# Optimization experiments

Hardware: AMD Instinct MI355X
Metric: run time of the kernel (lower is better)

## Reference

```python
import jax, jax.numpy as jnp
import numpy as np

EPS = 1e-10
N_NODES = 100000
OUT_CH = 128
N_EDGES = 625000


def setup_inputs() -> dict:
    key = jax.random.key(0)
    k_emb, k_eidx, k_enorm, k_lw, k_sw = jax.random.split(key, 5)
    emb = jax.random.normal(k_emb, (N_NODES, OUT_CH), dtype=jnp.float32) * 0.02
    edge_index = jax.random.randint(k_eidx, (2, N_EDGES), 0, N_NODES, dtype=jnp.int64)
    edge_norm = jax.random.uniform(k_enorm, (N_EDGES,), dtype=jnp.float32)
    scale = 1.0 / np.sqrt(OUT_CH)
    loc_w = jax.random.normal(k_lw, (OUT_CH, OUT_CH), dtype=jnp.float32) * scale
    loc_b = jnp.zeros((OUT_CH,), dtype=jnp.float32)
    std_w = jax.random.normal(k_sw, (OUT_CH, OUT_CH), dtype=jnp.float32) * scale
    std_b = jnp.zeros((OUT_CH,), dtype=jnp.float32)
    return {"emb": emb, "edge_index": edge_index, "edge_norm": edge_norm,
            "loc_w": loc_w, "loc_b": loc_b, "std_w": std_w, "std_b": std_b}


def reference(emb, edge_index, edge_norm, loc_w, loc_b, std_w, std_b):
    """GraphEncoder (GraphConv gather-scale-scatter + Linear loc/std) followed by
    GraphDecoder dot-product logits on the same edge list. Eval mode: z = loc."""
    sidx = edge_index[0]
    tidx = edge_index[1]
    # GraphConv: message = x[sidx] * enorm ; scatter_add into target nodes
    message = emb[sidx] * edge_norm[:, None]               # [E, C]
    ptr = jax.ops.segment_sum(message, tidx, num_segments=emb.shape[0])  # [N, C]
    # Encoder heads (torch Linear: x @ W.T + b)
    loc = ptr @ loc_w.T + loc_b                            # [N, C]
    std = jax.nn.softplus(ptr @ std_w.T + std_b) + EPS     # [N, C]
    z = loc  # eval-mode embedding
    # GraphDecoder: Bernoulli logits per edge
    logits = jnp.sum(z[sidx] * z[tidx], axis=1)            # [E]
    return loc, std, logits
```

## Files before the change

### kernel.cpp

```cpp
#include <hip/hip_runtime.h>

#define N_NODES 100000
#define OUT_CH  128
#define N_EDGES 625000
#define NB_SCAN 98
#define ROWD 68

typedef short short8 __attribute__((ext_vector_type(8)));
typedef float f32x4  __attribute__((ext_vector_type(4)));
typedef float f32x2  __attribute__((ext_vector_type(2)));
typedef unsigned u32x4 __attribute__((ext_vector_type(4)));

__device__ inline short f32_bf16(float f) {
    union { float f; unsigned u; } c{f};
    unsigned r = 0x7FFFu + ((c.u >> 16) & 1u);
    return (short)((c.u + r) >> 16);
}
__device__ inline unsigned pack_bf16x2(float lo, float hi) {
    return (unsigned)(unsigned short)f32_bf16(lo) |
           ((unsigned)(unsigned short)f32_bf16(hi) << 16);
}
__device__ inline float sp_fast(float x) {
    float e = __expf(-fabsf(x));
    return fmaxf(x, 0.f) + __logf(1.f + e);
}

#if defined(__has_builtin)
#if __has_builtin(__builtin_amdgcn_cvt_pk_f32_fp8) && __has_builtin(__builtin_amdgcn_cvt_pk_fp8_f32)
#define HWFP8 1
#endif
#endif
#ifndef HWFP8
#define HWFP8 0
#endif

__device__ inline unsigned f32_fp8_manual(float f) {
    union { float fl; unsigned u; } c{f};
    unsigned s = (c.u >> 31) << 7;
    float af = fabsf(f);
    if (!(af < 448.f)) return s | 0x7E;
    if (af < 0.015625f) {
        unsigned q = (unsigned)__float2int_rn(af * 512.f);
        return s | q;
    }
    unsigned u = c.u;
    u += 0x7FFFF + ((u >> 20) & 1);
    int e = (int)((u >> 23) & 255) - 127;
    if (e > 8) return s | 0x7E;
    return s | (((unsigned)(e + 7)) << 3) | ((u >> 20) & 7);
}
__device__ inline float fp8_f32_manual(unsigned b) {
    unsigned s = (b >> 7) & 1, e = (b >> 3) & 15, m = b & 7;
    if (e) { union { unsigned u; float f; } c{(s << 31) | ((e + 120) << 23) | (m << 20)}; return c.f; }
    float v = (float)m * 0.001953125f;
    return s ? -v : v;
}

template <bool HI>
__device__ inline f32x2 fp8x2_f32(unsigned v) {
#if HWFP8
    return __builtin_amdgcn_cvt_pk_f32_fp8((int)v, HI);
#else
    unsigned sh = HI ? 16 : 0;
    f32x2 r;
    r.x = fp8_f32_manual((v >> sh) & 0xff);
    r.y = fp8_f32_manual((v >> (sh + 8)) & 0xff);
    return r;
#endif
}
template <bool HI>
__device__ inline unsigned fp8_pack2(float a, float b, unsigned old) {
#if HWFP8
    return (unsigned)__builtin_amdgcn_cvt_pk_fp8_f32(a, b, (int)old, HI);
#else
    unsigned v = f32_fp8_manual(a) | (f32_fp8_manual(b) << 8);
    return HI ? ((old & 0x0000ffffu) | (v << 16)) : ((old & 0xffff0000u) | v);
#endif
}

#define NBB 16
#define NBE 6250
#define NBH 2442
__global__ void prep_all(const float* __restrict__ lw, const float* __restrict__ sw,
                         short8* __restrict__ B, const float4* __restrict__ emb,
                         uint2* __restrict__ embf8, const int* __restrict__ ei,
                         int* __restrict__ counts, int use_fp8) {
    int bid = blockIdx.x, tid = threadIdx.x;
    if (bid < NBB) {
        int g = bid * 256 + tid;
        int lane = g & 63, nt = (g >> 6) & 15, ks = g >> 10;
        int c = nt * 16 + (lane & 15);
        int k = ks * 32 + (lane >> 4) * 8;
        const float* src = (c < OUT_CH) ? (lw + c * OUT_CH + k)
                                        : (sw + (c - OUT_CH) * OUT_CH + k);
        short8 o;
#pragma unroll
        for (int j = 0; j < 8; ++j) o[j] = f32_bf16(src[j]);
        B[(ks * 16 + nt) * 64 + lane] = o;
    } else if (bid < NBB + NBE) {
        if (!use_fp8) return;
        int i = (bid - NBB) * 256 + tid;
        float4 a = emb[2 * i], b = emb[2 * i + 1];
        unsigned lo = fp8_pack2<false>(a.x * 64.f, a.y * 64.f, 0u);
        lo = fp8_pack2<true>(a.z * 64.f, a.w * 64.f, lo);
        unsigned hi = fp8_pack2<false>(b.x * 64.f, b.y * 64.f, 0u);
        hi = fp8_pack2<true>(b.z * 64.f, b.w * 64.f, hi);
        uint2 o; o.x = lo; o.y = hi;
        embf8[i] = o;
    } else {
        int e = (bid - NBB - NBE) * 256 + tid;
        if (e < N_EDGES) atomicAdd(&counts[ei[N_EDGES + e]], 1);
    }
}

__global__ void scan1_k(const int* __restrict__ counts, int* __restrict__ offsets,
                        int* __restrict__ partials, int* __restrict__ cursors) {
    __shared__ int wsum[16];
    int tid = threadIdx.x, lane = tid & 63, wid = tid >> 6;
    int e = blockIdx.x * 1024 + tid;
    int v = (e < N_NODES) ? counts[e] : 0;
    int incl = v;
#pragma unroll
    for (int d = 1; d < 64; d <<= 1) {
        int t = __shfl_up(incl, d);
        if (lane >= d) incl += t;
    }
    if (lane == 63) wsum[wid] = incl;
    __syncthreads();
    if (wid == 0) {
        int w = (lane < 16) ? wsum[lane] : 0;
        int wi = w;
#pragma unroll
        for (int d = 1; d < 16; d <<= 1) {
            int t = __shfl_up(wi, d);
            if (lane >= d) wi += t;
        }
        if (lane < 16) wsum[lane] = wi - w;
        if (lane == 15) partials[blockIdx.x] = wi;
    }
    __syncthreads();
    int excl = incl - v + wsum[wid];
    if (e < N_NODES) { offsets[e] = excl; cursors[e] = excl; }
}

__global__ void scan2_k(int* __restrict__ partials, int nb) {
    int lane = threadIdx.x;
    int i0 = 2 * lane, i1 = 2 * lane + 1;
    int v0 = (i0 < nb) ? partials[i0] : 0;
    int v1 = (i1 < nb) ? partials[i1] : 0;
    int s = v0 + v1;
    int incl = s;
#pragma unroll
    for (int d = 1; d < 64; d <<= 1) {
        int t = __shfl_up(incl, d);
        if (lane >= d) incl += t;
    }
    int excl = incl - s;
    if (i0 < nb) partials[i0] = excl;
    if (i1 < nb) partials[i1] = excl + v0;
}

__global__ void reorder_k(const int* __restrict__ ei, const float* __restrict__ en,
                          const int* __restrict__ partials, int* __restrict__ cursors,
                          int4* __restrict__ edata, float nscale) {
    int e = blockIdx.x * blockDim.x + threadIdx.x;
    if (e >= N_EDGES) return;
    int t = ei[N_EDGES + e];
    int pos = partials[t >> 10] + atomicAdd(&cursors[t], 1);
    int4 d;
    d.x = ei[e];
    d.y = __float_as_int(en[e] * nscale);
    d.z = e;
    d.w = t;
    edata[pos] = d;
}

__global__ __launch_bounds__(1024) void enc_fp8_k(
        const unsigned short* __restrict__ embf8,
        const int* __restrict__ offsets, const int* __restrict__ partials,
        const int4* __restrict__ edata, const short8* __restrict__ B,
        const float* __restrict__ lb, const float* __restrict__ sb,
        float* __restrict__ out, unsigned* __restrict__ zf8) {
    __shared__ unsigned lds[16 * ROWD];
    int tid = threadIdx.x, wid = tid >> 6, lane = tid & 63;
    int node = __builtin_amdgcn_readfirstlane(blockIdx.x * 16 + wid);

    int beg = offsets[node] + partials[node >> 10];
    int end = (node == N_NODES - 1) ? N_EDGES
              : offsets[node + 1] + partials[(node + 1) >> 10];
    float ax = 0.f, ay = 0.f;
    int j = beg;
    for (; j + 4 <= end; j += 4) {
        int4 p0 = edata[j], p1 = edata[j + 1], p2 = edata[j + 2], p3 = edata[j + 3];
        unsigned v0 = embf8[(size_t)p0.x * 64 + lane];
        unsigned v1 = embf8[(size_t)p1.x * 64 + lane];
        unsigned v2 = embf8[(size_t)p2.x * 64 + lane];
        unsigned v3 = embf8[(size_t)p3.x * 64 + lane];
        float n0f = __int_as_float(p0.y), n1f = __int_as_float(p1.y);
        float n2f = __int_as_float(p2.y), n3f = __int_as_float(p3.y);
        f32x2 d0 = fp8x2_f32<false>(v0), d1 = fp8x2_f32<false>(v1);
        f32x2 d2 = fp8x2_f32<false>(v2), d3 = fp8x2_f32<false>(v3);
        ax += d0.x * n0f + d1.x * n1f + d2.x * n2f + d3.x * n3f;
        ay += d0.y * n0f + d1.y * n1f + d2.y * n2f + d3.y * n3f;
    }
    for (; j < end; ++j) {
        int4 p = edata[j];
        float nm = __int_as_float(p.y);
        f32x2 d = fp8x2_f32<false>(embf8[(size_t)p.x * 64 + lane]);
        ax += d.x * nm; ay += d.y * nm;
    }
    lds[wid * ROWD + lane] = pack_bf16x2(ax, ay);
    __syncthreads();

    int arow = lane & 15, hi = lane >> 4;
    f32x4 acc = (f32x4)(0.f);
#pragma unroll
    for (int ks = 0; ks < 4; ++ks) {
        short8 a = *(const short8*)&lds[arow * ROWD + ks * 16 + hi * 4];
        short8 w = B[(ks * 16 + wid) * 64 + lane];
        acc = __builtin_amdgcn_mfma_f32_16x16x32_bf16(w, a, acc, 0, 0, 0);
    }
    int onode = blockIdx.x * 16 + arow;
    int ch4 = hi * 4;
    if (wid < 8) {
        int c = wid * 16 + ch4;
        float4 b4 = *(const float4*)(lb + c);
        float4 v;
        v.x = acc[0] + b4.x; v.y = acc[1] + b4.y;
        v.z = acc[2] + b4.z; v.w = acc[3] + b4.w;
        *(float4*)(out + (size_t)onode * OUT_CH + c) = v;
        unsigned zp = fp8_pack2<false>(v.x * 16.f, v.y * 16.f, 0u);
        zp = fp8_pack2<true>(v.z * 16.f, v.w * 16.f, zp);
        zf8[(size_t)onode * 32 + (c >> 2)] = zp;
    } else {
        int cc = (wid - 8) * 16 + ch4;
        float4 b4 = *(const float4*)(sb + cc);
        float4 v;
        v.x = sp_fast(acc[0] + b4.x) + 1e-10f;
        v.y = sp_fast(acc[1] + b4.y) + 1e-10f;
        v.z = sp_fast(acc[2] + b4.z) + 1e-10f;
        v.w = sp_fast(acc[3] + b4.w) + 1e-10f;
        *(float4*)(out + (size_t)N_NODES * OUT_CH + (size_t)onode * OUT_CH + cc) = v;
    }
}

__global__ void gather_f32_k(const float* __restrict__ emb,
                             const int* __restrict__ offsets,
                             const int* __restrict__ partials,
                             const int4* __restrict__ edata,
                             unsigned* __restrict__ ptrb) {
    int g = blockIdx.x * blockDim.x + threadIdx.x;
    int node = __builtin_amdgcn_readfirstlane(g >> 6);
    int lane = threadIdx.x & 63;
    if (node >= N_NODES) return;
    int beg = offsets[node] + partials[node >> 10];
    int end = (node == N_NODES - 1) ? N_EDGES
              : offsets[node + 1] + partials[(node + 1) >> 10];
    float ax = 0.f, ay = 0.f;
    const float2* base = (const float2*)emb;
    int j = beg;
    for (; j + 4 <= end; j += 4) {
        int4 p0 = edata[j], p1 = edata[j + 1], p2 = edata[j + 2], p3 = edata[j + 3];
        float2 v0 = base[(size_t)p0.x * 64 + lane];
        float2 v1 = base[(size_t)p1.x * 64 + lane];
        float2 v2 = base[(size_t)p2.x * 64 + lane];
        float2 v3 = base[(size_t)p3.x * 64 + lane];
        float n0f = __int_as_float(p0.y), n1f = __int_as_float(p1.y);
        float n2f = __int_as_float(p2.y), n3f = __int_as_float(p3.y);
        ax += v0.x * n0f + v1.x * n1f + v2.x * n2f + v3.x * n3f;
        ay += v0.y * n0f + v1.y * n1f + v2.y * n2f + v3.y * n3f;
    }
    for (; j < end; ++j) {
        int4 p = edata[j];
        float nm = __int_as_float(p.y);
        float2 v = base[(size_t)p.x * 64 + lane];
        ax += v.x * nm; ay += v.y * nm;
    }
    ptrb[(size_t)node * 64 + lane] = pack_bf16x2(ax, ay);
}

__global__ __launch_bounds__(256) void gemm_k(const short* __restrict__ P,
                                              float* __restrict__ out,
                                              const short8* __restrict__ B,
                                              const float* __restrict__ lb,
                                              const float* __restrict__ sb) {
    int tid = threadIdx.x;
    int wave = tid >> 6, lane = tid & 63;
    int n0 = (blockIdx.x * 4 + wave) * 16;
    if (n0 >= N_NODES) return;

    float* loc  = out;
    float* stdo = out + (size_t)N_NODES * OUT_CH;

    int prow = n0 + (lane & 15);
    int kb = (lane >> 4) * 8;

    f32x4 acc[16];
#pragma unroll
    for (int i = 0; i < 16; ++i) acc[i] = (f32x4)(0.f);

#pragma unroll
    for (int ks = 0; ks < 4; ++ks) {
        short8 a = *(const short8*)(P + (size_t)prow * OUT_CH + ks * 32 + kb);
#pragma unroll
        for (int nt = 0; nt < 16; ++nt) {
            short8 w = B[(ks * 16 + nt) * 64 + lane];
            acc[nt] = __builtin_amdgcn_mfma_f32_16x16x32_bf16(w, a, acc[nt], 0, 0, 0);
        }
    }

    int node = n0 + (lane & 15);
    int ch4 = (lane >> 4) * 4;
    float* lrow = loc  + (size_t)node * OUT_CH;
    float* srow = stdo + (size_t)node * OUT_CH;

#pragma unroll
    for (int nt = 0; nt < 8; ++nt) {
        int c = nt * 16 + ch4;
        float4 b4 = *(const float4*)(lb + c);
        float4 v;
        v.x = acc[nt][0] + b4.x; v.y = acc[nt][1] + b4.y;
        v.z = acc[nt][2] + b4.z; v.w = acc[nt][3] + b4.w;
        *(float4*)(lrow + c) = v;
    }
#pragma unroll
    for (int nt = 8; nt < 16; ++nt) {
        int cc = nt * 16 + ch4 - OUT_CH;
        float4 b4 = *(const float4*)(sb + cc);
        float4 v;
        v.x = sp_fast(acc[nt][0] + b4.x) + 1e-10f;
        v.y = sp_fast(acc[nt][1] + b4.y) + 1e-10f;
        v.z = sp_fast(acc[nt][2] + b4.z) + 1e-10f;
        v.w = sp_fast(acc[nt][3] + b4.w) + 1e-10f;
        *(float4*)(srow + cc) = v;
    }
}

__global__ void logits_fp8_k(const u32x4* __restrict__ zf8,
                             const int4* __restrict__ edata,
                             float* __restrict__ lg) {
    int idx = blockIdx.x * blockDim.x + threadIdx.x;
    int p = idx >> 3, q = idx & 7;
    if (p >= N_EDGES) return;
    int4 md = edata[p];
    u32x4 a = zf8[(size_t)md.x * 8 + q];
    u32x4 b = zf8[(size_t)md.w * 8 + q];
    float d = 0.f;
#pragma unroll
    for (int k = 0; k < 4; ++k) {
        f32x2 al = fp8x2_f32<false>(a[k]), ah = fp8x2_f32<true>(a[k]);
        f32x2 bl = fp8x2_f32<false>(b[k]), bh = fp8x2_f32<true>(b[k]);
        d += al.x * bl.x + al.y * bl.y + ah.x * bh.x + ah.y * bh.y;
    }
#pragma unroll
    for (int m = 4; m >= 1; m >>= 1) d += __shfl_xor(d, m);
    if (q == 0) lg[md.z] = d * 0.00390625f;
}

__global__ void logits_f32_k(const float* __restrict__ z, const int* __restrict__ ei,
                             float* __restrict__ lg) {
    int idx = blockIdx.x * blockDim.x + threadIdx.x;
    int e = idx >> 5, q = idx & 31;
    if (e >= N_EDGES) return;
    int s = ei[e], t = ei[N_EDGES + e];
    float4 a = *(const float4*)(z + (size_t)s * OUT_CH + q * 4);
    float4 b = *(const float4*)(z + (size_t)t * OUT_CH + q * 4);
    float d = a.x * b.x + a.y * b.y + a.z * b.z + a.w * b.w;
#pragma unroll
    for (int m = 16; m >= 1; m >>= 1) d += __shfl_xor(d, m);
    if (q == 0) lg[e] = d;
}

extern "C" void kernel_launch(void* const* d_in, const int* in_sizes, int n_in,
                              void* d_out, int out_size, void* d_ws, size_t ws_size,
                              hipStream_t stream) {
    const float* emb = (const float*)d_in[0];
    const int*   ei  = (const int*)d_in[1];
    const float* en  = (const float*)d_in[2];
    const float* lw  = (const float*)d_in[3];
    const float* lb  = (const float*)d_in[4];
    const float* sw  = (const float*)d_in[5];
    const float* sb  = (const float*)d_in[6];
    float* out = (float*)d_out;

    char* ws = (char*)d_ws;
    size_t o = 0;
    short8* B       = (short8*)(ws + o); o += 65536;
    int*    counts  = (int*)(ws + o);    o += 400128;
    int*    offsets = (int*)(ws + o);    o += 400128;
    int*    cursors = (int*)(ws + o);    o += 400128;
    int*    partials= (int*)(ws + o);    o += 1024;
    int4*   edata   = (int4*)(ws + o);   o += (size_t)N_EDGES * 16;
    unsigned* ptrb  = (unsigned*)(ws + o); o += (size_t)N_NODES * OUT_CH * 2;

    unsigned* zf8   = (unsigned*)(ws + o);
    unsigned short* embf8 = (unsigned short*)(ws + o + (size_t)N_NODES * OUT_CH);
    size_t o_end = o + (size_t)N_NODES * OUT_CH * 2;
    int use_fp8 = (o_end <= ws_size) ? 1 : 0;

    hipMemsetAsync(counts, 0, N_NODES * sizeof(int), stream);

    prep_all<<<NBB + NBE + NBH, 256, 0, stream>>>(lw, sw, B, (const float4*)emb,
                                                  (uint2*)embf8, ei, counts, use_fp8);
    scan1_k<<<NB_SCAN, 1024, 0, stream>>>(counts, offsets, partials, cursors);
    scan2_k<<<1, 64, 0, stream>>>(partials, NB_SCAN);
    reorder_k<<<(N_EDGES + 255) / 256, 256, 0, stream>>>(
        ei, en, partials, cursors, edata, use_fp8 ? 0.015625f : 1.0f);
    float* lg = out + (size_t)2 * N_NODES * OUT_CH;
    if (use_fp8) {
        enc_fp8_k<<<N_NODES / 16, 1024, 0, stream>>>(embf8, offsets, partials,
                                                     edata, B, lb, sb, out, zf8);
        logits_fp8_k<<<((size_t)N_EDGES * 8 + 255) / 256, 256, 0, stream>>>(
            (const u32x4*)zf8, edata, lg);
    } else {
        gather_f32_k<<<(N_NODES * 64 + 255) / 256, 256, 0, stream>>>(
            emb, offsets, partials, edata, ptrb);
        gemm_k<<<(N_NODES / 16 + 3) / 4, 256, 0, stream>>>((const short*)ptrb, out,
                                                           B, lb, sb);
        logits_f32_k<<<((size_t)N_EDGES * 32 + 255) / 256, 256, 0, stream>>>(out, ei, lg);
    }
}
```

Before: 177.0 us.

## Sort nodes by in-degree so encoder blocks process similar-degree nodes together

Builds a degree histogram during the scan, prefix-sums it, then scatters node IDs into degree-bucketed order. The fused encoder kernel now maps each wave to a node taken from this sorted list, so the 16 waves in a block have similar edge counts and finish at similar times before the shared MFMA step. The cost is an extra kernel, extra atomics, and output rows written in scattered order instead of contiguously.

```diff
diff --git a/kernel.cpp b/kernel.cpp
--- a/kernel.cpp
+++ b/kernel.cpp
@@ -114,11 +114,14 @@
 }
 
 __global__ void scan1_k(const int* __restrict__ counts, int* __restrict__ offsets,
-                        int* __restrict__ partials, int* __restrict__ cursors) {
+                        int* __restrict__ partials, int* __restrict__ cursors,
+                        int* __restrict__ dcur) {
     __shared__ int wsum[16];
+    __shared__ int lh[64];
     int tid = threadIdx.x, lane = tid & 63, wid = tid >> 6;
     int e = blockIdx.x * 1024 + tid;
     int v = (e < N_NODES) ? counts[e] : 0;
+    if (tid < 64) lh[tid] = 0;
     int incl = v;
 #pragma unroll
     for (int d = 1; d < 64; d <<= 1) {
@@ -127,6 +130,7 @@
     }
     if (lane == 63) wsum[wid] = incl;
     __syncthreads();
+    if (e < N_NODES) atomicAdd(&lh[v < 63 ? v : 63], 1);
     if (wid == 0) {
         int w = (lane < 16) ? wsum[lane] : 0;
         int wi = w;
@@ -141,9 +145,10 @@
     __syncthreads();
     int excl = incl - v + wsum[wid];
     if (e < N_NODES) { offsets[e] = excl; cursors[e] = excl; }
-}
-
-__global__ void scan2_k(int* __restrict__ partials, int nb) {
+    if (tid < 64 && lh[tid]) atomicAdd(&dcur[tid], lh[tid]);
+}
+
+__global__ void scan2_k(int* __restrict__ partials, int nb, int* __restrict__ dcur) {
     int lane = threadIdx.x;
     int i0 = 2 * lane, i1 = 2 * lane + 1;
     int v0 = (i0 < nb) ? partials[i0] : 0;
@@ -158,6 +163,25 @@
     int excl = incl - s;
     if (i0 < nb) partials[i0] = excl;
     if (i1 < nb) partials[i1] = excl + v0;
+
+    int dv = dcur[lane];
+    int di = dv;
+#pragma unroll
+    for (int d = 1; d < 64; d <<= 1) {
+        int t = __shfl_up(di, d);
+        if (lane >= d) di += t;
+    }
+    dcur[lane] = di - dv;
+}
+
+__global__ void dscatter_k(const int* __restrict__ counts, int* __restrict__ dcur,
+                           int* __restrict__ sorted) {
+    int n = blockIdx.x * blockDim.x + threadIdx.x;
+    if (n >= N_NODES) return;
+    int v = counts[n];
+    int b = v < 63 ? v : 63;
+    int pos = atomicAdd(&dcur[b], 1);
+    sorted[pos] = n;
 }
 
 __global__ void reorder_k(const int* __restrict__ ei, const float* __restrict__ en,
@@ -180,10 +204,11 @@
         const int* __restrict__ offsets, const int* __restrict__ partials,
         const int4* __restrict__ edata, const short8* __restrict__ B,
         const float* __restrict__ lb, const float* __restrict__ sb,
+        const int* __restrict__ sorted,
         float* __restrict__ out, unsigned* __restrict__ zf8) {
     __shared__ unsigned lds[16 * ROWD];
     int tid = threadIdx.x, wid = tid >> 6, lane = tid & 63;
-    int node = __builtin_amdgcn_readfirstlane(blockIdx.x * 16 + wid);
+    int node = __builtin_amdgcn_readfirstlane(sorted[blockIdx.x * 16 + wid]);
 
     int beg = offsets[node] + partials[node >> 10];
     int end = (node == N_NODES - 1) ? N_EDGES
@@ -220,7 +245,7 @@
         short8 w = B[(ks * 16 + wid) * 64 + lane];
         acc = __builtin_amdgcn_mfma_f32_16x16x32_bf16(w, a, acc, 0, 0, 0);
     }
-    int onode = blockIdx.x * 16 + arow;
+    int onode = sorted[blockIdx.x * 16 + arow];
     int ch4 = hi * 4;
     if (wid < 8) {
         int c = wid * 16 + ch4;
@@ -386,10 +411,12 @@
     char* ws = (char*)d_ws;
     size_t o = 0;
     short8* B       = (short8*)(ws + o); o += 65536;
-    int*    counts  = (int*)(ws + o);    o += 400128;
+    int*    counts  = (int*)(ws + o);    o += 400384;
+    int*    dcur    = (int*)((char*)counts + 400000);
     int*    offsets = (int*)(ws + o);    o += 400128;
     int*    cursors = (int*)(ws + o);    o += 400128;
     int*    partials= (int*)(ws + o);    o += 1024;
+    int*    sorted  = (int*)(ws + o);    o += 400128;
     int4*   edata   = (int4*)(ws + o);   o += (size_t)N_EDGES * 16;
     unsigned* ptrb  = (unsigned*)(ws + o); o += (size_t)N_NODES * OUT_CH * 2;
 
@@ -398,18 +425,20 @@
     size_t o_end = o + (size_t)N_NODES * OUT_CH * 2;
     int use_fp8 = (o_end <= ws_size) ? 1 : 0;
 
-    hipMemsetAsync(counts, 0, N_NODES * sizeof(int), stream);
+    hipMemsetAsync(counts, 0, 400384, stream);
 
     prep_all<<<NBB + NBE + NBH, 256, 0, stream>>>(lw, sw, B, (const float4*)emb,
                                                   (uint2*)embf8, ei, counts, use_fp8);
-    scan1_k<<<NB_SCAN, 1024, 0, stream>>>(counts, offsets, partials, cursors);
-    scan2_k<<<1, 64, 0, stream>>>(partials, NB_SCAN);
+    scan1_k<<<NB_SCAN, 1024, 0, stream>>>(counts, offsets, partials, cursors, dcur);
+    scan2_k<<<1, 64, 0, stream>>>(partials, NB_SCAN, dcur);
     reorder_k<<<(N_EDGES + 255) / 256, 256, 0, stream>>>(
         ei, en, partials, cursors, edata, use_fp8 ? 0.015625f : 1.0f);
+    dscatter_k<<<(N_NODES + 255) / 256, 256, 0, stream>>>(counts, dcur, sorted);
     float* lg = out + (size_t)2 * N_NODES * OUT_CH;
     if (use_fp8) {
         enc_fp8_k<<<N_NODES / 16, 1024, 0, stream>>>(embf8, offsets, partials,
-                                                     edata, B, lb, sb, out, zf8);
+                                                     edata, B, lb, sb, sorted,
+                                                     out, zf8);
         logits_fp8_k<<<((size_t)N_EDGES * 8 + 255) / 256, 256, 0, stream>>>(
             (const u32x4*)zf8, edata, lg);
     } else {
```

Measured after the change: 541.6 us. 206% more time.
